# Kernel optimization log

Measured on AMD Instinct MI355X. Metric: run time of the kernel, lower is better.

Reference implementation:

```python
import jax, jax.numpy as jnp
import numpy as np

B, T, D1, D2, DM, V, K = 2, 512, 256, 128, 1024, 32000, 4
SCALE = 0.05  # keep tanh/sigmoid out of full saturation with randn params


def setup_inputs() -> dict:
    key = jax.random.key(0)
    ks = jax.random.split(key, 7)
    s = lambda k, shape: SCALE * jax.random.normal(k, shape, dtype=jnp.float32)
    return {
        "gc": jax.random.normal(ks[0], (B, T, D1), dtype=jnp.float32),
        "H": s(ks[1], (K, DM, D1)),
        "U": s(ks[2], (K, D2, D1)),
        "v": s(ks[3], (V, D2)),
        "u": s(ks[4], (K, D1)),
        "b": s(ks[5], (V, K)),
        "emb": s(ks[6], (V, DM)),
    }


def reference(gc, H, U, v, u, b, emb):
    # gc: (B,T,D1)
    hc = jnp.tanh(jnp.einsum('kdi,bti->btkd', H, gc))        # (B,T,K,DM)
    tU = jnp.tanh(jnp.einsum('kji,bti->btkj', U, gc))        # (B,T,K,D2)
    # token- and context-dependent gate logits: (B,T,V,K)
    lc = (jnp.einsum('vj,btkj->btvk', v, tU)
          + jnp.einsum('ki,bti->btk', u, gc)[:, :, None, :]
          + b[None, None])
    gamma = jax.nn.sigmoid(lc[..., :K - 1])                  # (B,T,V,3)
    g0, g1, g2 = gamma[..., 0], gamma[..., 1], gamma[..., 2]
    # sigmoid-tree mixture priors: (B,T,V,K)
    pi = jnp.stack([g0 * g1, g0 * (1.0 - g1),
                    (1.0 - g0) * g2, (1.0 - g0) * (1.0 - g2)], axis=-1)
    # contract hc with embeddings per gate FIRST (avoids btikj blow-up),
    # then weight by pi -- same math as the original pi (x) emb outer product.
    dots = jnp.einsum('btkd,vd->btvk', hc, emb)              # (B,T,V,K)
    logits = jnp.sum(pi * dots, axis=-1)                     # (B,T,V)
    return jax.nn.softmax(logits, axis=-1)
```

## Files before the change

kernel.cpp:

```cpp
#include <hip/hip_runtime.h>
#include <math.h>

namespace {

typedef _Float16 f16;
typedef _Float16 f16x8 __attribute__((ext_vector_type(8)));
typedef float    f32x4 __attribute__((ext_vector_type(4)));

constexpr int kBT = 1024, kD1 = 256, kD2 = 128, kDM = 1024, kV = 32000, kK = 4;
constexpr int AR = kBT * kK;
constexpr int ROWS_H = kK * kDM;
constexpr int ROWS_U = kK * kD2;
constexpr int ROWS_ALL = ROWS_H + ROWS_U + kK;
constexpr int HALF_ROWS = ROWS_ALL / 2;
constexpr int NBY = kV / 128;

__global__ __launch_bounds__(256) void prep_gemm(
    const float* __restrict__ gc, const float* __restrict__ Hm,
    const float* __restrict__ Um, const float* __restrict__ um,
    f16* __restrict__ hc, f16* __restrict__ tu, float* __restrict__ ug)
{
    __shared__ float sgc[8][kD1];
    const int btBase = blockIdx.x * 8;
    for (int idx = threadIdx.x; idx < 8 * kD1; idx += 256)
        sgc[idx / kD1][idx % kD1] = gc[(size_t)btBase * kD1 + idx];
    __syncthreads();

    const int rStart = blockIdx.y * HALF_ROWS;
    const int rEnd   = rStart + HALF_ROWS;
    for (int r = rStart + (int)threadIdx.x; r < rEnd; r += 256) {
        const float* wrow;
        if (r < ROWS_H)               wrow = Hm + (size_t)r * kD1;
        else if (r < ROWS_H + ROWS_U) wrow = Um + (size_t)(r - ROWS_H) * kD1;
        else                          wrow = um + (size_t)(r - ROWS_H - ROWS_U) * kD1;

        float acc[8] = {0.f,0.f,0.f,0.f,0.f,0.f,0.f,0.f};
        for (int i = 0; i < kD1; i += 4) {
            const float4 w = *reinterpret_cast<const float4*>(wrow + i);
            #pragma unroll
            for (int b = 0; b < 8; ++b) {
                const float4 g = *reinterpret_cast<const float4*>(&sgc[b][i]);
                acc[b] = fmaf(w.x, g.x, acc[b]);
                acc[b] = fmaf(w.y, g.y, acc[b]);
                acc[b] = fmaf(w.z, g.z, acc[b]);
                acc[b] = fmaf(w.w, g.w, acc[b]);
            }
        }
        #pragma unroll
        for (int b = 0; b < 8; ++b) {
            const int bt = btBase + b;
            if (r < ROWS_H) {
                const int k = r >> 10, d = r & 1023;
                hc[((size_t)(bt * kK + k) << 10) + d] = (f16)tanhf(acc[b]);
            } else if (r < ROWS_H + ROWS_U) {
                const int r2 = r - ROWS_H;
                const int k = r2 >> 7, j = r2 & 127;
                tu[(size_t)(bt * kK + k) * kD2 + j] = (f16)tanhf(acc[b]);
            } else {
                ug[bt * kK + (r - ROWS_H - ROWS_U)] = acc[b];
            }
        }
    }
}

__global__ __launch_bounds__(256) void cvt_kernel(
    const float* __restrict__ src, f16* __restrict__ dst, int n8)
{
    const int i = blockIdx.x * 256 + threadIdx.x;
    if (i >= n8) return;
    const float4 x0 = *reinterpret_cast<const float4*>(src + (size_t)i * 8);
    const float4 x1 = *reinterpret_cast<const float4*>(src + (size_t)i * 8 + 4);
    union { f16 h[8]; uint4 v; } u;
    u.h[0] = (f16)x0.x; u.h[1] = (f16)x0.y; u.h[2] = (f16)x0.z; u.h[3] = (f16)x0.w;
    u.h[4] = (f16)x1.x; u.h[5] = (f16)x1.y; u.h[6] = (f16)x1.z; u.h[7] = (f16)x1.w;
    *reinterpret_cast<uint4*>(dst + (size_t)i * 8) = u.v;
}

__device__ __forceinline__ uint packf16x2(float a, float b) {
    union { f16 h[2]; uint u; } z;
    z.h[0] = (f16)a; z.h[1] = (f16)b;
    return z.u;
}

__global__ __launch_bounds__(512, 2) void fused_mfma(
    const f16* __restrict__ hc,  const f16* __restrict__ tu,
    const f16* __restrict__ v16, const f16* __restrict__ e16,
    const float* __restrict__ ug, const float* __restrict__ bmat,
    float* __restrict__ out, float* __restrict__ psum)
{
    __shared__ __align__(16) f16 sA[4][256 * 32];
    __shared__ __align__(16) f16 sB[4][128 * 32];

    const int tid  = threadIdx.x;
    const int lane = tid & 63;
    const int wave = tid >> 6;
    const int fr = lane & 15, fq = lane >> 4;
    const int wm = wave >> 1, wc = wave & 1;

    const int bx = blockIdx.x;
    const int by = blockIdx.y;
    const int aRowBase = bx * 256;
    const int vBase    = by * 128;
    const int btB      = bx * 64 + wm * 16;

    const int srowL = lane >> 2;
    const int scolL = ((lane & 3) ^ ((lane >> 3) & 3)) * 8;

    const int rslot = (fq ^ ((fr >> 1) & 3)) * 8;

    auto stage_any = [&](int g, bool gate) {
        const f16* A = gate ? tu : hc;
        const f16* B = gate ? v16 : e16;
        const int stride = gate ? kD2 : kDM;
        const int colb = (gate ? g : (g - 4)) * 32 + scolL;
        const int slot = g & 3;
        #pragma unroll
        for (int i = 0; i < 2; ++i) {
            const int c = wave * 2 + i;
            const f16* src = A + (size_t)(aRowBase + c * 16 + srowL) * stride + colb;
            __builtin_amdgcn_global_load_lds(
                (const __attribute__((address_space(1))) void*)src,
                (__attribute__((address_space(3))) void*)(&sA[slot][c * 512]), 16, 0, 0);
        }
        const f16* srcb = B + (size_t)(vBase + wave * 16 + srowL) * stride + colb;
        __builtin_amdgcn_global_load_lds(
            (const __attribute__((address_space(1))) void*)srcb,
            (__attribute__((address_space(3))) void*)(&sB[slot][wave * 512]), 16, 0, 0);
    };
    auto stage = [&](int g) { stage_any(g, g < 4); };
    auto stage_d = [&](int g) { stage_any(g, false); };

#define PHASE(G, ACC, DO_STAGE, STG_FN, VM)                                   \
    {                                                                         \
        const int slot_ = (G) & 3;                                            \
        const f16* __restrict__ pa_ = &sA[slot_][0];                          \
        const f16* __restrict__ pb_ = &sB[slot_][0];                          \
        f16x8 a_[4], b_[4];                                                   \
        _Pragma("unroll")                                                     \
        for (int m = 0; m < 4; ++m)                                           \
            a_[m] = *reinterpret_cast<const f16x8*>(                          \
                pa_ + (wm * 64 + m * 16 + fr) * 32 + rslot);                  \
        _Pragma("unroll")                                                     \
        for (int n = 0; n < 4; ++n)                                           \
            b_[n] = *reinterpret_cast<const f16x8*>(                          \
                pb_ + (wc * 64 + n * 16 + fr) * 32 + rslot);                  \
        if (DO_STAGE) STG_FN((G) + 3);                                        \
        asm volatile("s_waitcnt vmcnt(" VM ")" ::: "memory");                 \
        __builtin_amdgcn_s_barrier();                                         \
        asm volatile("" ::: "memory");                                        \
        __builtin_amdgcn_s_setprio(1);                                        \
        _Pragma("unroll")                                                     \
        for (int m = 0; m < 4; ++m)                                           \
            _Pragma("unroll")                                                 \
            for (int n = 0; n < 4; ++n)                                       \
                ACC[m][n] = __builtin_amdgcn_mfma_f32_16x16x32_f16(           \
                    a_[m], b_[n], ACC[m][n], 0, 0, 0);                        \
        __builtin_amdgcn_s_setprio(0);                                        \
        asm volatile("" ::: "memory");                                        \
        __builtin_amdgcn_s_barrier();                                         \
        asm volatile("" ::: "memory");                                        \
    }

    f32x4 acc[4][4];
    const f32x4 zz = {0.f, 0.f, 0.f, 0.f};
    #pragma unroll
    for (int m = 0; m < 4; ++m)
        #pragma unroll
        for (int n = 0; n < 4; ++n) acc[m][n] = zz;

    stage(0); stage(1); stage(2);
    asm volatile("s_waitcnt vmcnt(6)" ::: "memory");
    __builtin_amdgcn_s_barrier();
    asm volatile("" ::: "memory");

    PHASE(0, acc, true, stage, "6");
    PHASE(1, acc, true, stage, "6");

    float4 bb[4], ugv[4];
    #pragma unroll
    for (int n = 0; n < 4; ++n)
        bb[n] = *reinterpret_cast<const float4*>(
            bmat + (size_t)(vBase + wc * 64 + n * 16 + fr) * 4);
    #pragma unroll
    for (int m = 0; m < 4; ++m)
        ugv[m] = *reinterpret_cast<const float4*>(ug + (btB + m * 4 + fq) * 4);

    PHASE(2, acc, true, stage, "6");
    PHASE(3, acc, true, stage, "6");

    uint pi01[4][4], pi23[4][4];
    #pragma unroll
    for (int m = 0; m < 4; ++m) {
        #pragma unroll
        for (int n = 0; n < 4; ++n) {
            const float l0 = acc[m][n][0] + ugv[m].x + bb[n].x;
            const float l1 = acc[m][n][1] + ugv[m].y + bb[n].y;
            const float l2 = acc[m][n][2] + ugv[m].z + bb[n].z;
            const float g0 = 1.f / (1.f + __expf(-l0));
            const float g1 = 1.f / (1.f + __expf(-l1));
            const float g2 = 1.f / (1.f + __expf(-l2));
            pi01[m][n] = packf16x2(g0 * g1, g0 * (1.f - g1));
            pi23[m][n] = packf16x2((1.f - g0) * g2, (1.f - g0) * (1.f - g2));
        }
    }
    #pragma unroll
    for (int m = 0; m < 4; ++m)
        #pragma unroll
        for (int n = 0; n < 4; ++n) acc[m][n] = zz;

    for (int gg = 4; gg < 32; gg += 4) {
        PHASE(gg + 0, acc, true, stage_d, "6");
        PHASE(gg + 1, acc, true, stage_d, "6");
        PHASE(gg + 2, acc, true, stage_d, "6");
        PHASE(gg + 3, acc, true, stage_d, "6");
    }
    PHASE(32, acc, true,  stage_d, "6");
    PHASE(33, acc, false, stage_d, "3");
    PHASE(34, acc, false, stage_d, "0");
    PHASE(35, acc, false, stage_d, "0");
#undef PHASE

    #pragma unroll
    for (int m = 0; m < 4; ++m) {
        const int bt = btB + m * 4 + fq;
        float es = 0.f;
        #pragma unroll
        for (int n = 0; n < 4; ++n) {
            const int v = vBase + wc * 64 + n * 16 + fr;
            union { uint u; f16 h[2]; } p01, p23;
            p01.u = pi01[m][n]; p23.u = pi23[m][n];
            const float lg = (float)p01.h[0] * acc[m][n][0]
                           + (float)p01.h[1] * acc[m][n][1]
                           + (float)p23.h[0] * acc[m][n][2]
                           + (float)p23.h[1] * acc[m][n][3];
            out[(size_t)bt * kV + v] = lg;
            es += __expf(lg);
        }
        es += __shfl_xor(es, 1);
        es += __shfl_xor(es, 2);
        es += __shfl_xor(es, 4);
        es += __shfl_xor(es, 8);
        if (fr == 0)
            psum[(size_t)bt * 512 + by * 2 + wc] = es;
    }
}

__global__ __launch_bounds__(256) void softmax_kernel(
    float* __restrict__ out, const float* __restrict__ psum)
{
    __shared__ float red[4];
    const int bt = blockIdx.x;
    float* row = out + (size_t)bt * kV;
    const int tid = threadIdx.x;

    float s = 0.f;
    for (int i = tid; i < 2 * NBY; i += 256) s += psum[(size_t)bt * 512 + i];
    #pragma unroll
    for (int o = 1; o < 64; o <<= 1) s += __shfl_xor(s, o);
    if ((tid & 63) == 0) red[tid >> 6] = s;
    __syncthreads();
    s = red[0] + red[1] + red[2] + red[3];
    const float inv = 1.f / s;

    for (int i = tid * 4; i < kV; i += 1024) {
        const float4 x = *reinterpret_cast<const float4*>(row + i);
        float4 y;
        y.x = __expf(x.x) * inv;
        y.y = __expf(x.y) * inv;
        y.z = __expf(x.z) * inv;
        y.w = __expf(x.w) * inv;
        *reinterpret_cast<float4*>(row + i) = y;
    }
}

}

extern "C" void kernel_launch(void* const* d_in, const int* in_sizes, int n_in,
                              void* d_out, int out_size, void* d_ws, size_t ws_size,
                              hipStream_t stream)
{
    (void)in_sizes; (void)n_in; (void)out_size; (void)ws_size;
    const float* gc   = (const float*)d_in[0];
    const float* Hm   = (const float*)d_in[1];
    const float* Um   = (const float*)d_in[2];
    const float* vmat = (const float*)d_in[3];
    const float* um   = (const float*)d_in[4];
    const float* bmat = (const float*)d_in[5];
    const float* emb  = (const float*)d_in[6];
    float* out = (float*)d_out;

    size_t off = 0;
    auto take = [&](size_t bytes) -> char* {
        char* p = (char*)d_ws + off;
        off += (bytes + 255) & ~(size_t)255;
        return p;
    };
    f16*   hc   = (f16*)  take((size_t)AR * kDM * 2);
    f16*   tu   = (f16*)  take((size_t)AR * kD2 * 2);
    f16*   v16  = (f16*)  take((size_t)kV * kD2 * 2);
    f16*   e16  = (f16*)  take((size_t)kV * kDM * 2);
    float* ug   = (float*)take((size_t)AR * 4);
    float* psum = (float*)take((size_t)kBT * 512 * 4);

    prep_gemm<<<dim3(kBT / 8, 2), 256, 0, stream>>>(gc, Hm, Um, um, hc, tu, ug);
    cvt_kernel<<<(kV * kD2 / 8 + 255) / 256, 256, 0, stream>>>(vmat, v16, kV * kD2 / 8);
    cvt_kernel<<<(kV * kDM / 8 + 255) / 256, 256, 0, stream>>>(emb, e16, kV * kDM / 8);
    fused_mfma<<<dim3(AR / 256, NBY), 512, 0, stream>>>(
        hc, tu, v16, e16, ug, bmat, out, psum);
    softmax_kernel<<<dim3(kBT), 256, 0, stream>>>(out, psum);
}
```

Baseline: 600.4 us.

## Widen fused MFMA tile to 256 vocab columns with 8x4 per-wave fragments

The fused gate/dot GEMM block tile grows from 256x128 to 256x256 over the vocabulary, with the waves rearranged as 2x4 so each wave holds an 8x4 grid of MFMA accumulators. The LDS staging is rewritten around precomputed base pointers and compile-time slot and column offsets, and A fragments are now read from LDS one row-block at a time after the barrier rather than prefetched before it. The psum layout and the softmax reduction are updated for four partial sums per vocabulary tile. The goal is to halve global reloads of the A operand and raise MFMA work per LDS read. In exchange it doubles accumulator registers and B-tile LDS, which may lower occupancy at 512 threads per block, and it halves the grid size.

```diff
diff --git a/kernel.cpp b/kernel.cpp
--- a/kernel.cpp
+++ b/kernel.cpp
@@ -13,7 +13,7 @@
 constexpr int ROWS_U = kK * kD2;
 constexpr int ROWS_ALL = ROWS_H + ROWS_U + kK;
 constexpr int HALF_ROWS = ROWS_ALL / 2;
-constexpr int NBY = kV / 128;
+constexpr int NBY = kV / 256;
 
 __global__ __launch_bounds__(256) void prep_gemm(
     const float* __restrict__ gc, const float* __restrict__ Hm,
@@ -89,139 +89,139 @@
     float* __restrict__ out, float* __restrict__ psum)
 {
     __shared__ __align__(16) f16 sA[4][256 * 32];
-    __shared__ __align__(16) f16 sB[4][128 * 32];
+    __shared__ __align__(16) f16 sB[4][256 * 32];
 
     const int tid  = threadIdx.x;
     const int lane = tid & 63;
     const int wave = tid >> 6;
     const int fr = lane & 15, fq = lane >> 4;
-    const int wm = wave >> 1, wc = wave & 1;
+    const int wm = wave >> 2, wc = wave & 3;
 
     const int bx = blockIdx.x;
     const int by = blockIdx.y;
     const int aRowBase = bx * 256;
-    const int vBase    = by * 128;
-    const int btB      = bx * 64 + wm * 16;
+    const int vBase    = by * 256;
+    const int btB      = bx * 64 + wm * 32;
 
     const int srowL = lane >> 2;
     const int scolL = ((lane & 3) ^ ((lane >> 3) & 3)) * 8;
+    const int loffD = srowL * kDM + scolL;
+    const int loffG = srowL * kD2 + scolL;
+
+    const f16* pA = hc  + (size_t)aRowBase * kDM + loffD;
+    const f16* pB = e16 + (size_t)vBase    * kDM + loffD;
+    const f16* qA = tu  + (size_t)aRowBase * kD2 + loffG;
+    const f16* qB = v16 + (size_t)vBase    * kD2 + loffG;
+
+    f16* dA0 = &sA[0][0] + (wave * 2 + 0) * 512;
+    f16* dA1 = &sA[0][0] + (wave * 2 + 1) * 512;
+    f16* dB0 = &sB[0][0] + (wave * 2 + 0) * 512;
+    f16* dB1 = &sB[0][0] + (wave * 2 + 1) * 512;
 
     const int rslot = (fq ^ ((fr >> 1) & 3)) * 8;
-
-    auto stage_any = [&](int g, bool gate) {
-        const f16* A = gate ? tu : hc;
-        const f16* B = gate ? v16 : e16;
-        const int stride = gate ? kD2 : kDM;
-        const int colb = (gate ? g : (g - 4)) * 32 + scolL;
-        const int slot = g & 3;
-        #pragma unroll
-        for (int i = 0; i < 2; ++i) {
-            const int c = wave * 2 + i;
-            const f16* src = A + (size_t)(aRowBase + c * 16 + srowL) * stride + colb;
-            __builtin_amdgcn_global_load_lds(
-                (const __attribute__((address_space(1))) void*)src,
-                (__attribute__((address_space(3))) void*)(&sA[slot][c * 512]), 16, 0, 0);
-        }
-        const f16* srcb = B + (size_t)(vBase + wave * 16 + srowL) * stride + colb;
-        __builtin_amdgcn_global_load_lds(
-            (const __attribute__((address_space(1))) void*)srcb,
-            (__attribute__((address_space(3))) void*)(&sB[slot][wave * 512]), 16, 0, 0);
-    };
-    auto stage = [&](int g) { stage_any(g, g < 4); };
-    auto stage_d = [&](int g) { stage_any(g, false); };
-
-#define PHASE(G, ACC, DO_STAGE, STG_FN, VM)                                   \
+    const f16* rA = &sA[0][0] + (wm * 128 + fr) * 32 + rslot;
+    const f16* rB = &sB[0][0] + (wc * 64  + fr) * 32 + rslot;
+
+#define GLD(SRC, DST)                                                         \
+    __builtin_amdgcn_global_load_lds(                                         \
+        (const __attribute__((address_space(1))) void*)(SRC),                 \
+        (__attribute__((address_space(3))) void*)(DST), 16, 0, 0)
+
+#define STG(G) do {                                                           \
+        constexpr int SL_  = (G) & 3;                                         \
+        constexpr int COL_ = ((G) < 4 ? (G) : (G) - 4) * 32;                  \
+        constexpr int CS_  = ((G) < 4 ? kD2 : kDM) * 16;                      \
+        const f16* A_ = ((G) < 4 ? qA : pA) + COL_;                           \
+        const f16* B_ = ((G) < 4 ? qB : pB) + COL_;                           \
+        GLD(A_ + (wave * 2 + 0) * CS_, dA0 + SL_ * 8192);                     \
+        GLD(A_ + (wave * 2 + 1) * CS_, dA1 + SL_ * 8192);                     \
+        GLD(B_ + (wave * 2 + 0) * CS_, dB0 + SL_ * 8192);                     \
+        GLD(B_ + (wave * 2 + 1) * CS_, dB1 + SL_ * 8192);                     \
+    } while (0)
+
+#define PHASE(G, VM, DOSTG)                                                   \
     {                                                                         \
-        const int slot_ = (G) & 3;                                            \
-        const f16* __restrict__ pa_ = &sA[slot_][0];                          \
-        const f16* __restrict__ pb_ = &sB[slot_][0];                          \
-        f16x8 a_[4], b_[4];                                                   \
-        _Pragma("unroll")                                                     \
-        for (int m = 0; m < 4; ++m)                                           \
-            a_[m] = *reinterpret_cast<const f16x8*>(                          \
-                pa_ + (wm * 64 + m * 16 + fr) * 32 + rslot);                  \
-        _Pragma("unroll")                                                     \
-        for (int n = 0; n < 4; ++n)                                           \
-            b_[n] = *reinterpret_cast<const f16x8*>(                          \
-                pb_ + (wc * 64 + n * 16 + fr) * 32 + rslot);                  \
-        if (DO_STAGE) STG_FN((G) + 3);                                        \
+        DOSTG;                                                                \
         asm volatile("s_waitcnt vmcnt(" VM ")" ::: "memory");                 \
         __builtin_amdgcn_s_barrier();                                         \
         asm volatile("" ::: "memory");                                        \
+        constexpr int SL_ = (G) & 3;                                          \
+        f16x8 bfr_[4];                                                        \
+        _Pragma("unroll")                                                     \
+        for (int n = 0; n < 4; ++n)                                           \
+            bfr_[n] = *reinterpret_cast<const f16x8*>(                        \
+                rB + SL_ * 8192 + n * 512);                                   \
         __builtin_amdgcn_s_setprio(1);                                        \
         _Pragma("unroll")                                                     \
-        for (int m = 0; m < 4; ++m)                                           \
+        for (int m = 0; m < 8; ++m) {                                         \
+            const f16x8 afr_ = *reinterpret_cast<const f16x8*>(               \
+                rA + SL_ * 8192 + m * 512);                                   \
             _Pragma("unroll")                                                 \
             for (int n = 0; n < 4; ++n)                                       \
-                ACC[m][n] = __builtin_amdgcn_mfma_f32_16x16x32_f16(           \
-                    a_[m], b_[n], ACC[m][n], 0, 0, 0);                        \
+                acc[m][n] = __builtin_amdgcn_mfma_f32_16x16x32_f16(           \
+                    afr_, bfr_[n], acc[m][n], 0, 0, 0);                       \
+        }                                                                     \
         __builtin_amdgcn_s_setprio(0);                                        \
         asm volatile("" ::: "memory");                                        \
         __builtin_amdgcn_s_barrier();                                         \
         asm volatile("" ::: "memory");                                        \
     }
-
-    f32x4 acc[4][4];
+#define PH(G) PHASE(G, "8", STG((G) + 3))
+#define PH4(G) PH(G) PH((G) + 1) PH((G) + 2) PH((G) + 3)
+
+    f32x4 acc[8][4];
     const f32x4 zz = {0.f, 0.f, 0.f, 0.f};
     #pragma unroll
-    for (int m = 0; m < 4; ++m)
+    for (int m = 0; m < 8; ++m)
         #pragma unroll
         for (int n = 0; n < 4; ++n) acc[m][n] = zz;
 
-    stage(0); stage(1); stage(2);
-    asm volatile("s_waitcnt vmcnt(6)" ::: "memory");
-    __builtin_amdgcn_s_barrier();
-    asm volatile("" ::: "memory");
-
-    PHASE(0, acc, true, stage, "6");
-    PHASE(1, acc, true, stage, "6");
-
-    float4 bb[4], ugv[4];
+    STG(0); STG(1); STG(2);
+
+    PH4(0)
+
+    uint pi01[8][4], pi23[8][4];
+    {
+        float4 bb[4];
+        #pragma unroll
+        for (int n = 0; n < 4; ++n)
+            bb[n] = *reinterpret_cast<const float4*>(
+                bmat + (size_t)(vBase + wc * 64 + n * 16 + fr) * 4);
+        #pragma unroll
+        for (int m = 0; m < 8; ++m) {
+            const float4 ugv = *reinterpret_cast<const float4*>(
+                ug + (btB + m * 4 + fq) * 4);
+            #pragma unroll
+            for (int n = 0; n < 4; ++n) {
+                const float l0 = acc[m][n][0] + ugv.x + bb[n].x;
+                const float l1 = acc[m][n][1] + ugv.y + bb[n].y;
+                const float l2 = acc[m][n][2] + ugv.z + bb[n].z;
+                const float g0 = 1.f / (1.f + __expf(-l0));
+                const float g1 = 1.f / (1.f + __expf(-l1));
+                const float g2 = 1.f / (1.f + __expf(-l2));
+                pi01[m][n] = packf16x2(g0 * g1, g0 * (1.f - g1));
+                pi23[m][n] = packf16x2((1.f - g0) * g2, (1.f - g0) * (1.f - g2));
+            }
+        }
+    }
     #pragma unroll
-    for (int n = 0; n < 4; ++n)
-        bb[n] = *reinterpret_cast<const float4*>(
-            bmat + (size_t)(vBase + wc * 64 + n * 16 + fr) * 4);
+    for (int m = 0; m < 8; ++m)
+        #pragma unroll
+        for (int n = 0; n < 4; ++n) acc[m][n] = zz;
+
+    PH4(4) PH4(8) PH4(12) PH4(16) PH4(20) PH4(24) PH4(28)
+    PH(32)
+    PHASE(33, "4", (void)0)
+    PHASE(34, "0", (void)0)
+    PHASE(35, "0", (void)0)
+#undef PH4
+#undef PH
+#undef PHASE
+#undef STG
+#undef GLD
+
     #pragma unroll
-    for (int m = 0; m < 4; ++m)
-        ugv[m] = *reinterpret_cast<const float4*>(ug + (btB + m * 4 + fq) * 4);
-
-    PHASE(2, acc, true, stage, "6");
-    PHASE(3, acc, true, stage, "6");
-
-    uint pi01[4][4], pi23[4][4];
-    #pragma unroll
-    for (int m = 0; m < 4; ++m) {
-        #pragma unroll
-        for (int n = 0; n < 4; ++n) {
-            const float l0 = acc[m][n][0] + ugv[m].x + bb[n].x;
-            const float l1 = acc[m][n][1] + ugv[m].y + bb[n].y;
-            const float l2 = acc[m][n][2] + ugv[m].z + bb[n].z;
-            const float g0 = 1.f / (1.f + __expf(-l0));
-            const float g1 = 1.f / (1.f + __expf(-l1));
-            const float g2 = 1.f / (1.f + __expf(-l2));
-            pi01[m][n] = packf16x2(g0 * g1, g0 * (1.f - g1));
-            pi23[m][n] = packf16x2((1.f - g0) * g2, (1.f - g0) * (1.f - g2));
-        }
-    }
-    #pragma unroll
-    for (int m = 0; m < 4; ++m)
-        #pragma unroll
-        for (int n = 0; n < 4; ++n) acc[m][n] = zz;
-
-    for (int gg = 4; gg < 32; gg += 4) {
-        PHASE(gg + 0, acc, true, stage_d, "6");
-        PHASE(gg + 1, acc, true, stage_d, "6");
-        PHASE(gg + 2, acc, true, stage_d, "6");
-        PHASE(gg + 3, acc, true, stage_d, "6");
-    }
-    PHASE(32, acc, true,  stage_d, "6");
-    PHASE(33, acc, false, stage_d, "3");
-    PHASE(34, acc, false, stage_d, "0");
-    PHASE(35, acc, false, stage_d, "0");
-#undef PHASE
-
-    #pragma unroll
-    for (int m = 0; m < 4; ++m) {
+    for (int m = 0; m < 8; ++m) {
         const int bt = btB + m * 4 + fq;
         float es = 0.f;
         #pragma unroll
@@ -241,7 +241,7 @@
         es += __shfl_xor(es, 4);
         es += __shfl_xor(es, 8);
         if (fr == 0)
-            psum[(size_t)bt * 512 + by * 2 + wc] = es;
+            psum[(size_t)bt * 512 + by * 4 + wc] = es;
     }
 }
 
@@ -254,7 +254,7 @@
     const int tid = threadIdx.x;
 
     float s = 0.f;
-    for (int i = tid; i < 2 * NBY; i += 256) s += psum[(size_t)bt * 512 + i];
+    for (int i = tid; i < 4 * NBY; i += 256) s += psum[(size_t)bt * 512 + i];
     #pragma unroll
     for (int o = 1; o < 64; o <<= 1) s += __shfl_xor(s, o);
     if ((tid & 63) == 0) red[tid >> 6] = s;
```

After: 674.6 us. 1.12x slower.
